# Kernel tuning notes

Hardware: AMD Instinct MI355X
Metric: run time of the kernel (lower is better)

Reference implementation:

```python
import jax, jax.numpy as jnp
import numpy as np

FFT_NORM = 'forward'


def setup_inputs() -> dict:
    key = jax.random.key(0)
    ks = jax.random.split(key, 6)
    B, N, Cin, Cout, T, M = 16, 16384, 64, 64, 256, 2049  # M = modes//2+1 with modes=4096
    x = jax.random.normal(ks[0], (B, N, Cin), dtype=jnp.float32)
    t_emb = jax.random.normal(ks[1], (B, T), dtype=jnp.float32)
    scale = 1.0 / jnp.sqrt(jnp.float32(Cin))
    weights_real = jax.random.normal(ks[2], (M, Cin, Cout), dtype=jnp.float32) * scale
    weights_imag = jax.random.normal(ks[3], (M, Cin, Cout), dtype=jnp.float32) * scale
    dense_real_w = jax.random.normal(ks[4], (M, T), dtype=jnp.float32) * (1.0 / jnp.sqrt(jnp.float32(T)))
    dense_imag_w = jax.random.normal(ks[5], (M, T), dtype=jnp.float32) * (1.0 / jnp.sqrt(jnp.float32(T)))
    return {"x": x, "t_emb": t_emb, "weights_real": weights_real,
            "weights_imag": weights_imag, "dense_real_w": dense_real_w,
            "dense_imag_w": dense_imag_w}


def reference(x, t_emb, weights_real, weights_imag, dense_real_w, dense_imag_w):
    B, N, _ = x.shape
    M, _, Cout = weights_real.shape  # M = modes//2+1
    W = weights_real + 1j * weights_imag  # (M, Cin, Cout) complex64
    # FFT along the grid axis
    x_ft = jnp.fft.rfft(x, axis=-2, norm=FFT_NORM)  # (B, N//2+1, Cin) complex64
    # Time modulation: eqx Linear (bias-free) = t_emb @ W^T
    t_mod = (t_emb @ dense_real_w.T) + 1j * (t_emb @ dense_imag_w.T)  # (B, M)
    # Diagonal modulation + channel mix, exactly equal to the eye/einsum pair:
    # out[b,i,o] = t_mod[b,i] * sum_c x_ft[b,i,c] * W[i,c,o]
    out_trunc = jnp.einsum('bi,bic,ico->bio', t_mod, x_ft[:, :M, :], W)  # (B, M, Cout)
    out_ft = jnp.zeros((B, N // 2 + 1, Cout), dtype=jnp.complex64)
    out_ft = out_ft.at[:, :M, :].set(out_trunc)
    out = jnp.fft.irfft(out_ft, axis=-2, n=N, norm=FFT_NORM)  # (B, N, Cout) float32
    return out
```

## Files before the change

### kernel.cpp

```cpp
#include <hip/hip_runtime.h>
#include <math.h>

#define B_   16
#define N_   16384
#define H_   8192
#define LOGH 13
#define CIN  64
#define COUT 64
#define T_   256
#define M_   2049

__device__ __forceinline__ unsigned br13(unsigned v) {
  return __brev(v) >> 19;
}

__device__ __forceinline__ int SW(int n) {
  return (n & ~31) | ((n ^ (n >> 5) ^ (n >> 10)) & 31);
}

__device__ __forceinline__ void cmul(float ar, float ai, float br, float bi,
                                     float& rr, float& ri) {
  rr = ar * br - ai * bi;
  ri = ar * bi + ai * br;
}

__device__ __constant__ float C16[16] = {
  1.f, 0.92387953251f, 0.70710678119f, 0.38268343236f, 0.f, -0.38268343236f,
  -0.70710678119f, -0.92387953251f, -1.f, -0.92387953251f, -0.70710678119f,
  -0.38268343236f, 0.f, 0.38268343236f, 0.70710678119f, 0.92387953251f};
__device__ __constant__ float S16[16] = {
  0.f, 0.38268343236f, 0.70710678119f, 0.92387953251f, 1.f, 0.92387953251f,
  0.70710678119f, 0.38268343236f, 0.f, -0.38268343236f, -0.70710678119f,
  -0.92387953251f, -1.f, -0.92387953251f, -0.70710678119f, -0.38268343236f};

template <int SIGN, int S0>
__device__ __forceinline__ void group16(float* __restrict__ sre,
                                        float* __restrict__ sim, int tid) {
  const int lo = tid & ((1 << S0) - 1);
  const int hi = tid >> S0;
  const int base = (hi << (S0 + 4)) + lo;
  int pp[16];
  float xr[16], xi[16];
#pragma unroll
  for (int j = 0; j < 16; ++j) {
    pp[j] = SW(base + (j << S0));
    xr[j] = sre[pp[j]];
    xi[j] = sim[pp[j]];
  }
  float th = 6.283185307179586f * (float)lo / (float)(16 << S0);
  float sn, cs;
  __sincosf(th, &sn, &cs);
  float w1r = cs, w1i = (float)SIGN * sn;
  float w2r, w2i, w4r, w4i, w8r, w8i;
  cmul(w1r, w1i, w1r, w1i, w2r, w2i);
  cmul(w2r, w2i, w2r, w2i, w4r, w4i);
  cmul(w4r, w4i, w4r, w4i, w8r, w8i);
  {
#pragma unroll
    for (int j = 0; j < 16; j += 2) {
      float br, bi;
      cmul(xr[j + 1], xi[j + 1], w8r, w8i, br, bi);
      xr[j + 1] = xr[j] - br; xi[j + 1] = xi[j] - bi;
      xr[j] += br; xi[j] += bi;
    }
  }
  {
    float tr[2], ti[2];
    tr[0] = w4r; ti[0] = w4i;
    cmul(w4r, w4i, C16[4], (float)SIGN * S16[4], tr[1], ti[1]);
#pragma unroll
    for (int j = 0; j < 16; ++j) {
      if ((j & 2) == 0) {
        int jl = j & 1;
        float br, bi;
        cmul(xr[j + 2], xi[j + 2], tr[jl], ti[jl], br, bi);
        xr[j + 2] = xr[j] - br; xi[j + 2] = xi[j] - bi;
        xr[j] += br; xi[j] += bi;
      }
    }
  }
  {
    float tr[4], ti[4];
#pragma unroll
    for (int jl = 0; jl < 4; ++jl)
      cmul(w2r, w2i, C16[2 * jl], (float)SIGN * S16[2 * jl], tr[jl], ti[jl]);
#pragma unroll
    for (int j = 0; j < 16; ++j) {
      if ((j & 4) == 0) {
        int jl = j & 3;
        float br, bi;
        cmul(xr[j + 4], xi[j + 4], tr[jl], ti[jl], br, bi);
        xr[j + 4] = xr[j] - br; xi[j + 4] = xi[j] - bi;
        xr[j] += br; xi[j] += bi;
      }
    }
  }
  {
    float tr[8], ti[8];
#pragma unroll
    for (int jl = 0; jl < 8; ++jl)
      cmul(w1r, w1i, C16[jl], (float)SIGN * S16[jl], tr[jl], ti[jl]);
#pragma unroll
    for (int j = 0; j < 8; ++j) {
      float br, bi;
      cmul(xr[j + 8], xi[j + 8], tr[j], ti[j], br, bi);
      xr[j + 8] = xr[j] - br; xi[j + 8] = xi[j] - bi;
      xr[j] += br; xi[j] += bi;
    }
  }
#pragma unroll
  for (int j = 0; j < 16; ++j) {
    sre[pp[j]] = xr[j];
    sim[pp[j]] = xi[j];
  }
}

template <int SIGN>
__device__ __forceinline__ void stageD(float* __restrict__ sre,
                                       float* __restrict__ sim, int tid) {
  float th = 6.283185307179586f * (float)tid / 8192.0f;
  float sn, cs;
  __sincosf(th, &sn, &cs);
  float wtr = cs, wti = (float)SIGN * sn;
#pragma unroll
  for (int s = 0; s < 8; ++s) {
    float twr, twi;
    cmul(wtr, wti, C16[s], (float)SIGN * S16[s], twr, twi);
    int i0 = tid + 512 * s;
    int p0 = SW(i0), p1 = SW(i0 + 4096);
    float br, bi;
    cmul(sre[p1], sim[p1], twr, twi, br, bi);
    float ar = sre[p0], ai = sim[p0];
    sre[p0] = ar + br; sim[p0] = ai + bi;
    sre[p1] = ar - br; sim[p1] = ai - bi;
  }
}

__global__ __launch_bounds__(256) void tmod_kernel(
    const float* __restrict__ t_emb,
    const float* __restrict__ dwr, const float* __restrict__ dwi,
    float* __restrict__ tmr, float* __restrict__ tmi) {
  int wave = threadIdx.x >> 6;
  int lane = threadIdx.x & 63;
  int p = blockIdx.x * 4 + wave;
  if (p >= B_ * M_) return;
  int b = p / M_, i = p % M_;
  float ar = 0.f, ai = 0.f;
  for (int j = 0; j < 4; ++j) {
    int t = lane + 64 * j;
    float te = t_emb[b * T_ + t];
    ar += te * dwr[(size_t)i * T_ + t];
    ai += te * dwi[(size_t)i * T_ + t];
  }
  for (int off = 32; off > 0; off >>= 1) {
    ar += __shfl_down(ar, off, 64);
    ai += __shfl_down(ai, off, 64);
  }
  if (lane == 0) { tmr[b * M_ + i] = ar; tmi[b * M_ + i] = ai; }
}

__global__ __launch_bounds__(256) void pack_transpose(
    const float* __restrict__ x, float* __restrict__ zre, float* __restrict__ zim) {
  __shared__ float tile[64][65];
  int b = blockIdx.y, nt = blockIdx.x;
  int n0 = nt * 64;
  int j  = threadIdx.x & 63;
  int iy = threadIdx.x >> 6;
  for (int p = 0; p < 16; ++p) {
    int i = iy + 4 * p;
    tile[i][j] = x[((size_t)(b * N_ + n0 + i)) * CIN + j];
  }
  __syncthreads();
  int ii = threadIdx.x & 31;
  int cy = threadIdx.x >> 5;
  int h0 = nt * 32;
  for (int p = 0; p < 8; ++p) {
    int c = cy + 8 * p;
    size_t o = (size_t)(b * CIN + c) * H_ + h0 + ii;
    zre[o] = tile[2 * ii][c];
    zim[o] = tile[2 * ii + 1][c];
  }
}

__global__ __launch_bounds__(512, 4) void fft_fwd(
    const float* __restrict__ zre, const float* __restrict__ zim,
    float* __restrict__ Xtr, float* __restrict__ Xti) {
  __shared__ float sre[H_], sim[H_];
  int hw = blockIdx.x;
  int bc = ((hw & 7) << 7) | (hw >> 3);
  int tid = threadIdx.x;
  size_t base = (size_t)bc * H_;
#pragma unroll
  for (int s = 0; s < 16; ++s) {
    int n = tid + 512 * s;
    int r = SW((int)br13(n));
    sre[r] = zre[base + n];
    sim[r] = zim[base + n];
  }
  __syncthreads();
  group16<-1, 0>(sre, sim, tid); __syncthreads();
  group16<-1, 4>(sre, sim, tid); __syncthreads();
  group16<-1, 8>(sre, sim, tid); __syncthreads();
  stageD<-1>(sre, sim, tid);     __syncthreads();
  const float sc = 1.0f / (float)N_;
  for (int k = tid; k < M_; k += 512) {
    int mk = (H_ - k) & (H_ - 1);
    int pk = SW(k), pm = SW(mk);
    float zr = sre[pk], zi = sim[pk];
    float mr = sre[pm], mi = -sim[pm];
    float Er = 0.5f * (zr + mr), Ei = 0.5f * (zi + mi);
    float Dr = zr - mr,          Di = zi - mi;
    float Or = 0.5f * Di,        Oi = -0.5f * Dr;
    float ang = -6.283185307179586f * (float)k / (float)N_;
    float sn, cs;
    __sincosf(ang, &sn, &cs);
    float Xr = Er + cs * Or - sn * Oi;
    float Xi = Ei + cs * Oi + sn * Or;
    Xtr[(size_t)k * 1024 + bc] = Xr * sc;
    Xti[(size_t)k * 1024 + bc] = Xi * sc;
  }
}

typedef short  s8v  __attribute__((ext_vector_type(8)));
typedef float  f4v  __attribute__((ext_vector_type(4)));

__device__ __forceinline__ unsigned short f2bf_hi(float x) {
  unsigned u = __float_as_uint(x);
  unsigned r = (u + 0x7fffu + ((u >> 16) & 1u)) >> 16;
  return (unsigned short)r;
}

__device__ __forceinline__ int fbi(int k, int n) {
  return ((((n >> 4) * 2 + (k >> 5)) << 9) | (((n & 15) + (((k >> 3) & 3) << 4)) << 3) | (k & 7));
}
__device__ __forceinline__ int fai(int k, int m) {
  return (((k >> 5) << 9) | (((m & 15) + (((k >> 3) & 3) << 4)) << 3) | (k & 7));
}

__global__ __launch_bounds__(256) void mix_mfma(
    const float* __restrict__ Xtr, const float* __restrict__ Xti,
    const float* __restrict__ Wr_g, const float* __restrict__ Wi_g,
    const float* __restrict__ tmr, const float* __restrict__ tmi,
    float* __restrict__ Ytr, float* __restrict__ Yti) {
  __shared__ __align__(16) unsigned short BrH[4096], BrL[4096], BiH[4096], BiL[4096];
  __shared__ __align__(16) unsigned short ArH[1024], ArL[1024];
  __shared__ __align__(16) unsigned short AiH[1024], AiL[1024];
  __shared__ __align__(16) unsigned short AnH[1024], AnL[1024];
  __shared__ float tms[32];
  const int hw = blockIdx.x;
  const int i  = (hw & 7) * 257 + (hw >> 3);
  if ((hw >> 3) >= 257 || i >= M_) return;
  const int tid = threadIdx.x;

  const float4* wr4 = (const float4*)(Wr_g + (size_t)i * 4096);
  const float4* wi4 = (const float4*)(Wi_g + (size_t)i * 4096);
#pragma unroll
  for (int it = 0; it < 4; ++it) {
    int f4 = it * 256 + tid;
    float4 vr = wr4[f4];
    float4 vi = wi4[f4];
    int idx0 = f4 * 4;
    float er[4] = {vr.x, vr.y, vr.z, vr.w};
    float ei[4] = {vi.x, vi.y, vi.z, vi.w};
#pragma unroll
    for (int e = 0; e < 4; ++e) {
      int idx = idx0 + e;
      int k = idx >> 6, n = idx & 63;
      int a = fbi(k, n);
      unsigned short h = f2bf_hi(er[e]);
      float hf = __uint_as_float(((unsigned)h) << 16);
      BrH[a] = h; BrL[a] = f2bf_hi(er[e] - hf);
      h = f2bf_hi(ei[e]);
      hf = __uint_as_float(((unsigned)h) << 16);
      BiH[a] = h; BiL[a] = f2bf_hi(ei[e] - hf);
    }
  }
  {
    float4 vr = ((const float4*)(Xtr + (size_t)i * 1024))[tid];
    float4 vi = ((const float4*)(Xti + (size_t)i * 1024))[tid];
    float er[4] = {vr.x, vr.y, vr.z, vr.w};
    float ei[4] = {vi.x, vi.y, vi.z, vi.w};
    int idx0 = tid * 4;
#pragma unroll
    for (int e = 0; e < 4; ++e) {
      int idx = idx0 + e;
      int m = idx >> 6, k = idx & 63;
      int a = fai(k, m);
      unsigned short h = f2bf_hi(er[e]);
      float hf = __uint_as_float(((unsigned)h) << 16);
      ArH[a] = h; ArL[a] = f2bf_hi(er[e] - hf);
      h = f2bf_hi(ei[e]);
      hf = __uint_as_float(((unsigned)h) << 16);
      unsigned short l = f2bf_hi(ei[e] - __uint_as_float(((unsigned)h) << 16));
      AiH[a] = h; AiL[a] = l;
      AnH[a] = h ^ 0x8000u; AnL[a] = l ^ 0x8000u;
    }
  }
  if (tid < 16) {
    tms[tid]      = tmr[tid * M_ + i];
    tms[16 + tid] = tmi[tid * M_ + i];
  }
  __syncthreads();

  const int w = tid >> 6, L = tid & 63;
  const s8v* pArH = (const s8v*)ArH; const s8v* pArL = (const s8v*)ArL;
  const s8v* pAiH = (const s8v*)AiH; const s8v* pAiL = (const s8v*)AiL;
  const s8v* pAnH = (const s8v*)AnH; const s8v* pAnL = (const s8v*)AnL;
  const s8v* pBrH = (const s8v*)BrH; const s8v* pBrL = (const s8v*)BrL;
  const s8v* pBiH = (const s8v*)BiH; const s8v* pBiL = (const s8v*)BiL;

  f4v cr = {0.f, 0.f, 0.f, 0.f}, ci = {0.f, 0.f, 0.f, 0.f};
#pragma unroll
  for (int s = 0; s < 2; ++s) {
    s8v arh = pArH[s * 64 + L], arl = pArL[s * 64 + L];
    s8v aih = pAiH[s * 64 + L], ail = pAiL[s * 64 + L];
    s8v anh = pAnH[s * 64 + L], anl = pAnL[s * 64 + L];
    int bo = (w * 2 + s) * 64 + L;
    s8v brh = pBrH[bo], brl = pBrL[bo];
    s8v bih = pBiH[bo], bil = pBiL[bo];
    cr = __builtin_amdgcn_mfma_f32_16x16x32_bf16(arh, brh, cr, 0, 0, 0);
    cr = __builtin_amdgcn_mfma_f32_16x16x32_bf16(arh, brl, cr, 0, 0, 0);
    cr = __builtin_amdgcn_mfma_f32_16x16x32_bf16(arl, brh, cr, 0, 0, 0);
    cr = __builtin_amdgcn_mfma_f32_16x16x32_bf16(anh, bih, cr, 0, 0, 0);
    cr = __builtin_amdgcn_mfma_f32_16x16x32_bf16(anh, bil, cr, 0, 0, 0);
    cr = __builtin_amdgcn_mfma_f32_16x16x32_bf16(anl, bih, cr, 0, 0, 0);
    ci = __builtin_amdgcn_mfma_f32_16x16x32_bf16(arh, bih, ci, 0, 0, 0);
    ci = __builtin_amdgcn_mfma_f32_16x16x32_bf16(arh, bil, ci, 0, 0, 0);
    ci = __builtin_amdgcn_mfma_f32_16x16x32_bf16(arl, bih, ci, 0, 0, 0);
    ci = __builtin_amdgcn_mfma_f32_16x16x32_bf16(aih, brh, ci, 0, 0, 0);
    ci = __builtin_amdgcn_mfma_f32_16x16x32_bf16(aih, brl, ci, 0, 0, 0);
    ci = __builtin_amdgcn_mfma_f32_16x16x32_bf16(ail, brh, ci, 0, 0, 0);
  }

  const int n = (L & 15) + 16 * w;
  const int quad = L >> 4;
#pragma unroll
  for (int r = 0; r < 4; ++r) {
    int m = quad * 4 + r;
    float tr = tms[m], ti = tms[16 + m];
    float yr = tr * cr[r] - ti * ci[r];
    float yi = tr * ci[r] + ti * cr[r];
    size_t o = (size_t)(m * 64 + n) * M_ + i;
    Ytr[o] = yr;
    Yti[o] = yi;
  }
}

__global__ __launch_bounds__(512, 4) void fft_inv(
    const float* __restrict__ Ytr, const float* __restrict__ Yti,
    float* __restrict__ zre, float* __restrict__ zim) {
  __shared__ float sre[H_], sim[H_];
  int bo = blockIdx.x;
  int tid = threadIdx.x;
  size_t ybase = (size_t)bo * M_;
#pragma unroll
  for (int s = 0; s < 16; ++s) {
    int k = tid + 512 * s;
    float ykr = 0.f, yki = 0.f, ymr = 0.f, ymi = 0.f;
    if (k < M_) { ykr = Ytr[ybase + k]; yki = Yti[ybase + k]; }
    int m = H_ - k;
    if (m < M_) { ymr = Ytr[ybase + m]; ymi = -Yti[ybase + m]; }
    float Sr = ykr + ymr, Si = yki + ymi;
    float Dr = ykr - ymr, Di = yki - ymi;
    float ang = 6.283185307179586f * (float)k / (float)N_;
    float sn, cs;
    __sincosf(ang, &sn, &cs);
    float Zr = Sr - (cs * Di + sn * Dr);
    float Zi = Si + (cs * Dr - sn * Di);
    int r = SW((int)br13(k));
    sre[r] = Zr; sim[r] = Zi;
  }
  __syncthreads();
  group16<1, 0>(sre, sim, tid); __syncthreads();
  group16<1, 4>(sre, sim, tid); __syncthreads();
  group16<1, 8>(sre, sim, tid); __syncthreads();
  stageD<1>(sre, sim, tid);     __syncthreads();
  size_t base = (size_t)bo * H_;
#pragma unroll
  for (int s = 0; s < 16; ++s) {
    int n = tid + 512 * s;
    int p = SW(n);
    zre[base + n] = sre[p];
    zim[base + n] = sim[p];
  }
}

__global__ __launch_bounds__(256) void unpack_transpose(
    const float* __restrict__ zre, const float* __restrict__ zim,
    float* __restrict__ out) {
  __shared__ float tre[64][33], tim[64][33];
  int b = blockIdx.y, ht = blockIdx.x;
  int h0 = ht * 32;
  int ii = threadIdx.x & 31, cy = threadIdx.x >> 5;
  for (int p = 0; p < 8; ++p) {
    int c = cy + 8 * p;
    size_t idx = (size_t)(b * COUT + c) * H_ + h0 + ii;
    tre[c][ii] = zre[idx];
    tim[c][ii] = zim[idx];
  }
  __syncthreads();
  int o = threadIdx.x & 63, ry = threadIdx.x >> 6;
  for (int p = 0; p < 16; ++p) {
    int r = ry + 4 * p;
    int n = h0 * 2 + r;
    float v = (r & 1) ? tim[o][r >> 1] : tre[o][r >> 1];
    out[((size_t)(b * N_ + n)) * COUT + o] = v;
  }
}

extern "C" void kernel_launch(void* const* d_in, const int* in_sizes, int n_in,
                              void* d_out, int out_size, void* d_ws, size_t ws_size,
                              hipStream_t stream) {
  const float* x    = (const float*)d_in[0];
  const float* temb = (const float*)d_in[1];
  const float* wr   = (const float*)d_in[2];
  const float* wi   = (const float*)d_in[3];
  const float* dwr  = (const float*)d_in[4];
  const float* dwi  = (const float*)d_in[5];
  float* out = (float*)d_out;

  float* ws  = (float*)d_ws;
  float* tmr = ws;
  float* tmi = tmr + 32784;
  float* zre = tmi + 32784;
  float* zim = zre + 8388608;
  float* Xtr = zim + 8388608;
  float* Xti = Xtr + 2098176;
  float* Ytr = Xti + 2098176;
  float* Yti = Ytr + 2098176;

  tmod_kernel<<<dim3((B_ * M_ + 3) / 4), 256, 0, stream>>>(temb, dwr, dwi, tmr, tmi);
  pack_transpose<<<dim3(N_ / 64, B_), 256, 0, stream>>>(x, zre, zim);
  fft_fwd<<<dim3(B_ * CIN), 512, 0, stream>>>(zre, zim, Xtr, Xti);
  mix_mfma<<<dim3(2056), 256, 0, stream>>>(Xtr, Xti, wr, wi, tmr, tmi, Ytr, Yti);
  fft_inv<<<dim3(B_ * COUT), 512, 0, stream>>>(Ytr, Yti, zre, zim);
  unpack_transpose<<<dim3(H_ / 32, B_), 256, 0, stream>>>(zre, zim, out);
}
```

Measured before the change: 304.9 us.

## Assign one frequency mode per wave and load MFMA operands directly from global memory

The mixing kernel now has each wavefront own a whole frequency mode instead of one block per mode. The A and B fragments are loaded straight from global memory into registers and split into bf16 hi/lo pairs there, so the LDS staging and the block barrier go away. The grid shrinks from 2056 to 520 blocks. Weight loads now use strided scalar reads (stride 64 floats) with less coalescing, and there are fewer waves to hide latency.

Measured after the change: 308.3 us. No clear change (+1.1%).

```diff
diff --git a/kernel.cpp b/kernel.cpp
--- a/kernel.cpp
+++ b/kernel.cpp
@@ -229,12 +229,14 @@
   unsigned r = (u + 0x7fffu + ((u >> 16) & 1u)) >> 16;
   return (unsigned short)r;
 }
-
-__device__ __forceinline__ int fbi(int k, int n) {
-  return ((((n >> 4) * 2 + (k >> 5)) << 9) | (((n & 15) + (((k >> 3) & 3) << 4)) << 3) | (k & 7));
-}
-__device__ __forceinline__ int fai(int k, int m) {
-  return (((k >> 5) << 9) | (((m & 15) + (((k >> 3) & 3) << 4)) << 3) | (k & 7));
+__device__ __forceinline__ void cvt8(const float* v, s8v& h, s8v& l) {
+#pragma unroll
+  for (int e = 0; e < 8; ++e) {
+    unsigned short hh = f2bf_hi(v[e]);
+    float hf = __uint_as_float(((unsigned)hh) << 16);
+    h[e] = (short)hh;
+    l[e] = (short)f2bf_hi(v[e] - hf);
+  }
 }
 
 __global__ __launch_bounds__(256) void mix_mfma(
@@ -242,107 +244,79 @@
     const float* __restrict__ Wr_g, const float* __restrict__ Wi_g,
     const float* __restrict__ tmr, const float* __restrict__ tmi,
     float* __restrict__ Ytr, float* __restrict__ Yti) {
-  __shared__ __align__(16) unsigned short BrH[4096], BrL[4096], BiH[4096], BiL[4096];
-  __shared__ __align__(16) unsigned short ArH[1024], ArL[1024];
-  __shared__ __align__(16) unsigned short AiH[1024], AiL[1024];
-  __shared__ __align__(16) unsigned short AnH[1024], AnL[1024];
-  __shared__ float tms[32];
   const int hw = blockIdx.x;
-  const int i  = (hw & 7) * 257 + (hw >> 3);
-  if ((hw >> 3) >= 257 || i >= M_) return;
-  const int tid = threadIdx.x;
-
-  const float4* wr4 = (const float4*)(Wr_g + (size_t)i * 4096);
-  const float4* wi4 = (const float4*)(Wi_g + (size_t)i * 4096);
-#pragma unroll
-  for (int it = 0; it < 4; ++it) {
-    int f4 = it * 256 + tid;
-    float4 vr = wr4[f4];
-    float4 vi = wi4[f4];
-    int idx0 = f4 * 4;
-    float er[4] = {vr.x, vr.y, vr.z, vr.w};
-    float ei[4] = {vi.x, vi.y, vi.z, vi.w};
-#pragma unroll
-    for (int e = 0; e < 4; ++e) {
-      int idx = idx0 + e;
-      int k = idx >> 6, n = idx & 63;
-      int a = fbi(k, n);
-      unsigned short h = f2bf_hi(er[e]);
-      float hf = __uint_as_float(((unsigned)h) << 16);
-      BrH[a] = h; BrL[a] = f2bf_hi(er[e] - hf);
-      h = f2bf_hi(ei[e]);
-      hf = __uint_as_float(((unsigned)h) << 16);
-      BiH[a] = h; BiL[a] = f2bf_hi(ei[e] - hf);
-    }
-  }
-  {
-    float4 vr = ((const float4*)(Xtr + (size_t)i * 1024))[tid];
-    float4 vi = ((const float4*)(Xti + (size_t)i * 1024))[tid];
-    float er[4] = {vr.x, vr.y, vr.z, vr.w};
-    float ei[4] = {vi.x, vi.y, vi.z, vi.w};
-    int idx0 = tid * 4;
-#pragma unroll
-    for (int e = 0; e < 4; ++e) {
-      int idx = idx0 + e;
-      int m = idx >> 6, k = idx & 63;
-      int a = fai(k, m);
-      unsigned short h = f2bf_hi(er[e]);
-      float hf = __uint_as_float(((unsigned)h) << 16);
-      ArH[a] = h; ArL[a] = f2bf_hi(er[e] - hf);
-      h = f2bf_hi(ei[e]);
-      hf = __uint_as_float(((unsigned)h) << 16);
-      unsigned short l = f2bf_hi(ei[e] - __uint_as_float(((unsigned)h) << 16));
-      AiH[a] = h; AiL[a] = l;
-      AnH[a] = h ^ 0x8000u; AnL[a] = l ^ 0x8000u;
-    }
-  }
-  if (tid < 16) {
-    tms[tid]      = tmr[tid * M_ + i];
-    tms[16 + tid] = tmi[tid * M_ + i];
-  }
-  __syncthreads();
-
-  const int w = tid >> 6, L = tid & 63;
-  const s8v* pArH = (const s8v*)ArH; const s8v* pArL = (const s8v*)ArL;
-  const s8v* pAiH = (const s8v*)AiH; const s8v* pAiL = (const s8v*)AiL;
-  const s8v* pAnH = (const s8v*)AnH; const s8v* pAnL = (const s8v*)AnL;
-  const s8v* pBrH = (const s8v*)BrH; const s8v* pBrL = (const s8v*)BrL;
-  const s8v* pBiH = (const s8v*)BiH; const s8v* pBiL = (const s8v*)BiL;
-
-  f4v cr = {0.f, 0.f, 0.f, 0.f}, ci = {0.f, 0.f, 0.f, 0.f};
+  const int w  = threadIdx.x >> 6, L = threadIdx.x & 63;
+  const int il = (hw >> 3) * 4 + w;
+  if (il >= 257) return;
+  const int i = (hw & 7) * 257 + il;
+  if (i >= M_) return;
+  const int q = L >> 4, mlane = L & 15;
+
+  s8v arh[2], arl[2], aih[2], ail[2], anh[2], anl[2];
 #pragma unroll
   for (int s = 0; s < 2; ++s) {
-    s8v arh = pArH[s * 64 + L], arl = pArL[s * 64 + L];
-    s8v aih = pAiH[s * 64 + L], ail = pAiL[s * 64 + L];
-    s8v anh = pAnH[s * 64 + L], anl = pAnL[s * 64 + L];
-    int bo = (w * 2 + s) * 64 + L;
-    s8v brh = pBrH[bo], brl = pBrL[bo];
-    s8v bih = pBiH[bo], bil = pBiL[bo];
-    cr = __builtin_amdgcn_mfma_f32_16x16x32_bf16(arh, brh, cr, 0, 0, 0);
-    cr = __builtin_amdgcn_mfma_f32_16x16x32_bf16(arh, brl, cr, 0, 0, 0);
-    cr = __builtin_amdgcn_mfma_f32_16x16x32_bf16(arl, brh, cr, 0, 0, 0);
-    cr = __builtin_amdgcn_mfma_f32_16x16x32_bf16(anh, bih, cr, 0, 0, 0);
-    cr = __builtin_amdgcn_mfma_f32_16x16x32_bf16(anh, bil, cr, 0, 0, 0);
-    cr = __builtin_amdgcn_mfma_f32_16x16x32_bf16(anl, bih, cr, 0, 0, 0);
-    ci = __builtin_amdgcn_mfma_f32_16x16x32_bf16(arh, bih, ci, 0, 0, 0);
-    ci = __builtin_amdgcn_mfma_f32_16x16x32_bf16(arh, bil, ci, 0, 0, 0);
-    ci = __builtin_amdgcn_mfma_f32_16x16x32_bf16(arl, bih, ci, 0, 0, 0);
-    ci = __builtin_amdgcn_mfma_f32_16x16x32_bf16(aih, brh, ci, 0, 0, 0);
-    ci = __builtin_amdgcn_mfma_f32_16x16x32_bf16(aih, brl, ci, 0, 0, 0);
-    ci = __builtin_amdgcn_mfma_f32_16x16x32_bf16(ail, brh, ci, 0, 0, 0);
-  }
-
-  const int n = (L & 15) + 16 * w;
-  const int quad = L >> 4;
+    const float* xr = Xtr + (size_t)i * 1024 + mlane * 64 + q * 8 + 32 * s;
+    const float* xi = Xti + (size_t)i * 1024 + mlane * 64 + q * 8 + 32 * s;
+    float ar[8], ai_[8];
+    *(float4*)(ar)      = *(const float4*)(xr);
+    *(float4*)(ar + 4)  = *(const float4*)(xr + 4);
+    *(float4*)(ai_)     = *(const float4*)(xi);
+    *(float4*)(ai_ + 4) = *(const float4*)(xi + 4);
+    cvt8(ar, arh[s], arl[s]);
+    cvt8(ai_, aih[s], ail[s]);
+#pragma unroll
+    for (int e = 0; e < 8; ++e) {
+      anh[s][e] = (short)(((unsigned short)aih[s][e]) ^ 0x8000u);
+      anl[s][e] = (short)(((unsigned short)ail[s][e]) ^ 0x8000u);
+    }
+  }
+  float trm[4], tim_[4];
 #pragma unroll
   for (int r = 0; r < 4; ++r) {
-    int m = quad * 4 + r;
-    float tr = tms[m], ti = tms[16 + m];
-    float yr = tr * cr[r] - ti * ci[r];
-    float yi = tr * ci[r] + ti * cr[r];
-    size_t o = (size_t)(m * 64 + n) * M_ + i;
-    Ytr[o] = yr;
-    Yti[o] = yi;
+    int m = q * 4 + r;
+    trm[r]  = tmr[m * M_ + i];
+    tim_[r] = tmi[m * M_ + i];
+  }
+
+#pragma unroll
+  for (int nt = 0; nt < 4; ++nt) {
+    const int n = mlane + 16 * nt;
+    f4v cr = {0.f, 0.f, 0.f, 0.f}, ci = {0.f, 0.f, 0.f, 0.f};
+#pragma unroll
+    for (int s = 0; s < 2; ++s) {
+      const float* wrp = Wr_g + (size_t)i * 4096 + (q * 8 + 32 * s) * 64 + n;
+      const float* wip = Wi_g + (size_t)i * 4096 + (q * 8 + 32 * s) * 64 + n;
+      float brf[8], bif[8];
+#pragma unroll
+      for (int j = 0; j < 8; ++j) {
+        brf[j] = wrp[j * 64];
+        bif[j] = wip[j * 64];
+      }
+      s8v brh, brl, bih, bil;
+      cvt8(brf, brh, brl);
+      cvt8(bif, bih, bil);
+      cr = __builtin_amdgcn_mfma_f32_16x16x32_bf16(arh[s], brh, cr, 0, 0, 0);
+      cr = __builtin_amdgcn_mfma_f32_16x16x32_bf16(arh[s], brl, cr, 0, 0, 0);
+      cr = __builtin_amdgcn_mfma_f32_16x16x32_bf16(arl[s], brh, cr, 0, 0, 0);
+      cr = __builtin_amdgcn_mfma_f32_16x16x32_bf16(anh[s], bih, cr, 0, 0, 0);
+      cr = __builtin_amdgcn_mfma_f32_16x16x32_bf16(anh[s], bil, cr, 0, 0, 0);
+      cr = __builtin_amdgcn_mfma_f32_16x16x32_bf16(anl[s], bih, cr, 0, 0, 0);
+      ci = __builtin_amdgcn_mfma_f32_16x16x32_bf16(arh[s], bih, ci, 0, 0, 0);
+      ci = __builtin_amdgcn_mfma_f32_16x16x32_bf16(arh[s], bil, ci, 0, 0, 0);
+      ci = __builtin_amdgcn_mfma_f32_16x16x32_bf16(arl[s], bih, ci, 0, 0, 0);
+      ci = __builtin_amdgcn_mfma_f32_16x16x32_bf16(aih[s], brh, ci, 0, 0, 0);
+      ci = __builtin_amdgcn_mfma_f32_16x16x32_bf16(aih[s], brl, ci, 0, 0, 0);
+      ci = __builtin_amdgcn_mfma_f32_16x16x32_bf16(ail[s], brh, ci, 0, 0, 0);
+    }
+#pragma unroll
+    for (int r = 0; r < 4; ++r) {
+      int m = q * 4 + r;
+      float yr = trm[r] * cr[r] - tim_[r] * ci[r];
+      float yi = trm[r] * ci[r] + tim_[r] * cr[r];
+      size_t o = (size_t)(m * 64 + n) * M_ + i;
+      Ytr[o] = yr;
+      Yti[o] = yi;
+    }
   }
 }
 
@@ -432,7 +406,7 @@
   tmod_kernel<<<dim3((B_ * M_ + 3) / 4), 256, 0, stream>>>(temb, dwr, dwi, tmr, tmi);
   pack_transpose<<<dim3(N_ / 64, B_), 256, 0, stream>>>(x, zre, zim);
   fft_fwd<<<dim3(B_ * CIN), 512, 0, stream>>>(zre, zim, Xtr, Xti);
-  mix_mfma<<<dim3(2056), 256, 0, stream>>>(Xtr, Xti, wr, wi, tmr, tmi, Ytr, Yti);
+  mix_mfma<<<dim3(520), 256, 0, stream>>>(Xtr, Xti, wr, wi, tmr, tmi, Ytr, Yti);
   fft_inv<<<dim3(B_ * COUT), 512, 0, stream>>>(Ytr, Yti, zre, zim);
   unpack_transpose<<<dim3(H_ / 32, B_), 256, 0, stream>>>(zre, zim, out);
 }
```
